# Optimization experiments

Measured on AMD Instinct MI355X. Metric: run time of the kernel, lower is better.

The kernel has to match this reference:

```python
import jax, jax.numpy as jnp
import numpy as np

C = 19          # EEG channels
NP = C * C      # 361 channel pairs
D = 256         # UNIFIED_FEATURE_DIM
H = 8           # num_heads
HD = D // H     # head dim


def _build_mask():
    # rel[p, q] = True iff key-pair q shares a channel with query-pair p
    idx = np.arange(NP)
    ci, cj = idx // C, idx % C
    rel = ((ci[:, None] == ci[None, :]) | (ci[:, None] == cj[None, :]) |
           (cj[:, None] == ci[None, :]) | (cj[:, None] == cj[None, :]))
    return jnp.asarray(rel.reshape(C, C, NP))  # (channel_i, j, key_pair)

MASK = _build_mask()


def setup_inputs() -> dict:
    key = jax.random.key(0)
    ks = jax.random.split(key, 6)
    s = 0.05
    return {
        "x": jax.random.normal(ks[0], (32, NP, D), jnp.float32),
        # 19 stacked nn.MultiheadAttention modules: in_proj (3D, D) = [Wq; Wk; Wv]
        "w_in": jax.random.normal(ks[1], (C, 3 * D, D), jnp.float32) * s,
        "b_in": jnp.zeros((C, 3 * D), jnp.float32),
        "w_out": jax.random.normal(ks[2], (C, D, D), jnp.float32) * s,
        "b_out": jnp.zeros((C, D), jnp.float32),
        # fusion: nn.Linear(D, D)
        "w_fuse": jax.random.normal(ks[3], (D, D), jnp.float32) * s,
        "b_fuse": jnp.zeros((D,), jnp.float32),
    }


def reference(x, w_in, b_in, w_out, b_out, w_fuse, b_fuse):
    # x: (B, 361, D). Pair p=(i,j) at index i*19+j uses attention module i,
    # query = x[:, p], keys/values = pairs sharing channel i or j (mask).
    B = x.shape[0]
    wq, wk, wv = w_in[:, :D], w_in[:, D:2 * D], w_in[:, 2 * D:]
    bq, bk, bv = b_in[:, :D], b_in[:, D:2 * D], b_in[:, 2 * D:]

    # Per-channel K/V projections over all 361 pairs: (C, B, NP, D)
    K = jnp.einsum('bnd,ced->cbne', x, wk) + bk[:, None, None, :]
    V = jnp.einsum('bnd,ced->cbne', x, wv) + bv[:, None, None, :]
    # Queries grouped by first channel i: x reshaped to (B, C, C, D)
    xq = x.reshape(B, C, C, D)
    Q = jnp.einsum('bcjd,ced->cbje', xq, wq) + bq[:, None, None, :]  # (C,B,C,D)

    Qh = Q.reshape(C, B, C, H, HD)
    Kh = K.reshape(C, B, NP, H, HD)
    Vh = V.reshape(C, B, NP, H, HD)

    scale = 1.0 / jnp.sqrt(jnp.asarray(HD, x.dtype))
    scores = jnp.einsum('cbqhe,cbkhe->cbhqk', Qh, Kh) * scale  # (C,B,H,C,NP)
    scores = jnp.where(MASK[:, None, None, :, :], scores, -jnp.inf)
    attn = jax.nn.softmax(scores, axis=-1)

    out = jnp.einsum('cbhqk,cbkhe->cbqhe', attn, Vh).reshape(C, B, C, D)
    out = jnp.einsum('cbqd,ced->cbqe', out, w_out) + b_out[:, None, None, :]
    out = out.transpose(1, 0, 2, 3).reshape(B, NP, D)  # back to (B, 361, D)

    # fusion ('linear') + residual
    return out @ w_fuse.T + b_fuse + x
```

## Files before the change

### kernel.cpp

```cpp
#include <hip/hip_runtime.h>

#define CC 19
#define NPOS 361
#define NPAD 384
#define DIM 256
#define TKEY 32
#define NTILES 12

#define LDS_BYTES 67584

using bf16x8 = __attribute__((ext_vector_type(8))) short;
using f16x4  = __attribute__((ext_vector_type(4))) _Float16;
using floatx4 = __attribute__((ext_vector_type(4))) float;
using uintx2 = __attribute__((ext_vector_type(2))) unsigned int;

__device__ __forceinline__ unsigned short f2bf(float f) {
  unsigned u = __builtin_bit_cast(unsigned, f);
  u += 0x7fffu + ((u >> 16) & 1u);
  return (unsigned short)(u >> 16);
}

__device__ __forceinline__ float bf2f(unsigned short h) {
  return __builtin_bit_cast(float, ((unsigned)h) << 16);
}

__device__ __forceinline__ f16x4 pack4h(float a, float b, float c2, float d) {
  const auto h01 = __builtin_amdgcn_cvt_pkrtz(a, b);
  const auto h23 = __builtin_amdgcn_cvt_pkrtz(c2, d);
  uintx2 uv = {__builtin_bit_cast(unsigned, h01), __builtin_bit_cast(unsigned, h23)};
  return __builtin_bit_cast(f16x4, uv);
}

__device__ __forceinline__ void gload_lds16(const void* g, void* l) {
  __builtin_amdgcn_global_load_lds(
      (const __attribute__((address_space(1))) void*)g,
      (__attribute__((address_space(3))) void*)l, 16, 0, 0);
}

__global__ void conv_all_kernel(const float* __restrict__ x,
                                const float* __restrict__ w_in,
                                const float* __restrict__ w_fuse,
                                unsigned short* __restrict__ ws) {
  const int j = blockIdx.x * 256 + threadIdx.x;
  float4 v = make_float4(0.f, 0.f, 0.f, 0.f);
  unsigned short* dst;
  if (j < 786432) {
    const int row = j >> 6;
    const int off = (j & 63) << 2;
    const int b = row / NPAD;
    const int r = row - b * NPAD;
    if (r < NPOS) v = *(const float4*)&x[(b * NPOS + r) * DIM + off];
    dst = &ws[row * DIM + off];
  } else if (j < 1720320) {
    const int k = j - 786432;
    v = *(const float4*)&w_in[k << 2];
    dst = &ws[3145728 + (k << 2)];
  } else {
    const int k = j - 1720320;
    v = *(const float4*)&w_fuse[k << 2];
    dst = &ws[8126464 + (k << 2)];
  }
  ushort4 o;
  o.x = f2bf(v.x); o.y = f2bf(v.y); o.z = f2bf(v.z); o.w = f2bf(v.w);
  *(ushort4*)dst = o;
}

__launch_bounds__(512)
__global__ void wcomb_kernel(const float* __restrict__ wof,
                             const unsigned short* __restrict__ wfbf,
                             unsigned short* __restrict__ wcbf) {
  const int c = blockIdx.x >> 2;
  const int fslab = blockIdx.x & 3;
  const int tid = threadIdx.x;
  const int w = tid >> 6;
  const int lane = tid & 63;
  const int quad = lane >> 4;
  const int l16 = lane & 15;

  const int f_w = fslab * 64 + (w & 3) * 16;
  const int d0_w = (w >> 2) * 128;
  const floatx4 fzero = {0.f, 0.f, 0.f, 0.f};

  floatx4 acc[8];
#pragma unroll
  for (int nt = 0; nt < 8; ++nt) acc[nt] = fzero;

  for (int kt = 0; kt < 8; ++kt) {
    const bf16x8 a8 = *(const bf16x8*)&wfbf[(f_w + l16) * 256 + kt * 32 + quad * 8];
#pragma unroll
    for (int nt = 0; nt < 8; ++nt) {
      const int d = d0_w + nt * 16 + l16;
      bf16x8 bn;
#pragma unroll
      for (int j = 0; j < 8; ++j) {
        const float v = wof[c * 65536 + (kt * 32 + quad * 8 + j) * 256 + d];
        bn[j] = (short)f2bf(v);
      }
      acc[nt] = __builtin_amdgcn_mfma_f32_16x16x32_bf16(a8, bn, acc[nt], 0, 0, 0);
    }
  }
#pragma unroll
  for (int nt = 0; nt < 8; ++nt)
#pragma unroll
    for (int r = 0; r < 4; ++r)
      wcbf[(c * 256 + f_w + quad * 4 + r) * 256 + d0_w + nt * 16 + l16] =
          f2bf(acc[nt][r]);
}

__launch_bounds__(256, 2)
__global__ void attn_kernel(const float* __restrict__ b_in,
                            const unsigned short* __restrict__ xbf,
                            const unsigned short* __restrict__ wibf,
                            float* __restrict__ out) {
  const int bid = blockIdx.x;
  const int xcd = bid & 7;
  const int slot = bid >> 3;
  const int c = slot >> 3;
  const int p = ((slot & 7) << 3) | xcd;
  const int b = p >> 1;
  const int hb = p & 1;

  const int tid = threadIdx.x;
  const int w = tid >> 6;
  const int lane = tid & 63;
  const int quad = lane >> 4;
  const int l16 = lane & 15;
  const int eh = (hb * 4 + w) * 32;

  extern __shared__ char smem[];
  char* sx = smem;
  unsigned* msk = (unsigned*)(smem + 65536);
  float* sL = (float*)(smem + 67072);

  const float scale = 0.25503486f;
  const floatx4 fzero = {0.f, 0.f, 0.f, 0.f};

  const int xw = (l16 & 7) << 4;
  const size_t xrowbytes = (size_t)b * NPAD * 512;

#pragma unroll
  for (int u = 0; u < 2; ++u) {
#pragma unroll
    for (int call = 0; call < 4; ++call) {
      const int sbyte = w * 4096 + call * 1024 + (lane << 4);
      const int row = sbyte >> 9;
      const int inner = (sbyte & 511) ^ ((row & 7) << 4);
      gload_lds16((const char*)xbf + xrowbytes + (size_t)(u * TKEY + row) * 512 + inner,
                  sx + u * 16384 + w * 4096 + call * 1024);
    }
  }

  f16x4 qf[2][2];
  {
    bf16x8 wq[2][8];
#pragma unroll
    for (int m4 = 0; m4 < 2; ++m4)
#pragma unroll
      for (int k = 0; k < 8; ++k)
        wq[m4][k] = *(const bf16x8*)&wibf[(c * 768 + eh + m4 * 16 + l16) * DIM + k * 32 + quad * 8];
    float bq[2][4];
#pragma unroll
    for (int m4 = 0; m4 < 2; ++m4) {
      const float4 bv4 = *(const float4*)&b_in[c * 768 + eh + m4 * 16 + quad * 4];
      bq[m4][0] = bv4.x; bq[m4][1] = bv4.y; bq[m4][2] = bv4.z; bq[m4][3] = bv4.w;
    }
#pragma unroll
    for (int mt = 0; mt < 2; ++mt) {
      const int xrow = b * NPAD + c * CC + mt * 16 + l16;
      bf16x8 xq[8];
#pragma unroll
      for (int k = 0; k < 8; ++k)
        xq[k] = *(const bf16x8*)&xbf[xrow * DIM + k * 32 + quad * 8];
#pragma unroll
      for (int m4 = 0; m4 < 2; ++m4) {
        floatx4 acc = fzero;
#pragma unroll
        for (int k = 0; k < 8; ++k)
          acc = __builtin_amdgcn_mfma_f32_16x16x32_bf16(wq[m4][k], xq[k], acc, 0, 0, 0);
        qf[mt][m4] = pack4h((acc[0] + bq[m4][0]) * scale, (acc[1] + bq[m4][1]) * scale,
                            (acc[2] + bq[m4][2]) * scale, (acc[3] + bq[m4][3]) * scale);
      }
    }
  }

  bf16x8 wk[2][8], wv[2][8];
#pragma unroll
  for (int m4 = 0; m4 < 2; ++m4)
#pragma unroll
    for (int k = 0; k < 8; ++k) {
      wk[m4][k] =
          *(const bf16x8*)&wibf[(c * 768 + 256 + eh + m4 * 16 + l16) * DIM + k * 32 + quad * 8];
      wv[m4][k] =
          *(const bf16x8*)&wibf[(c * 768 + 512 + eh + m4 * 16 + l16) * DIM + k * 32 + quad * 8];
    }
  float bV[2];
#pragma unroll
  for (int ne = 0; ne < 2; ++ne) bV[ne] = b_in[c * 768 + 512 + eh + ne * 16 + l16];

  for (int e2 = tid; e2 < 384; e2 += 256) {
    const int q = e2 / 12;
    const int wd = e2 - q * 12;
    unsigned m = 0u;
    for (int i = 0; i < 32; ++i) {
      const int kabs = wd * 32 + i;
      const unsigned ki = ((unsigned)kabs * 110377u) >> 21;
      const unsigned kj = (unsigned)kabs - ki * 19u;
      if (kabs < NPOS && (ki == (unsigned)c || kj == (unsigned)c ||
                          ki == (unsigned)q || kj == (unsigned)q))
        m |= (1u << i);
    }
    msk[e2] = m;
  }

  floatx4 o_acc[2][2];
  float lsum[2] = {0.f, 0.f};
#pragma unroll
  for (int mt = 0; mt < 2; ++mt)
#pragma unroll
    for (int ne = 0; ne < 2; ++ne) o_acc[mt][ne] = fzero;

  __syncthreads();

  for (int s6 = 0; s6 < 6; ++s6) {
    const int tb = s6 * 2;
    if (s6 < 5) {
#pragma unroll
      for (int u = 0; u < 2; ++u) {
        const int t = tb + 2 + u;
        char* bxn = sx + (t & 3) * 16384;
#pragma unroll
        for (int call = 0; call < 4; ++call) {
          const int sbyte = w * 4096 + call * 1024 + (lane << 4);
          const int row = sbyte >> 9;
          const int inner = (sbyte & 511) ^ ((row & 7) << 4);
          gload_lds16((const char*)xbf + xrowbytes + (size_t)(t * TKEY + row) * 512 + inner,
                      bxn + w * 4096 + call * 1024);
        }
      }
    }

#pragma unroll
    for (int u = 0; u < 2; ++u) {
      const int t = tb + u;
      const char* bx = sx + (t & 3) * 16384;

      floatx4 aK[2][2], aV[2][2];
#pragma unroll
      for (int i = 0; i < 2; ++i)
#pragma unroll
        for (int j = 0; j < 2; ++j) { aK[i][j] = fzero; aV[i][j] = fzero; }
      __builtin_amdgcn_s_setprio(1);
#pragma unroll
      for (int k = 0; k < 8; ++k) {
        bf16x8 xfr[2];
#pragma unroll
        for (int n4 = 0; n4 < 2; ++n4) {
          const int row = n4 * 16 + l16;
          const int inner = (k * 64 + quad * 16) ^ xw;
          xfr[n4] = *(const bf16x8*)(bx + row * 512 + inner);
        }
#pragma unroll
        for (int m4 = 0; m4 < 2; ++m4)
#pragma unroll
          for (int n4 = 0; n4 < 2; ++n4) {
            aK[m4][n4] = __builtin_amdgcn_mfma_f32_16x16x32_bf16(wk[m4][k], xfr[n4], aK[m4][n4], 0, 0, 0);
            aV[n4][m4] = __builtin_amdgcn_mfma_f32_16x16x32_bf16(xfr[n4], wv[m4][k], aV[n4][m4], 0, 0, 0);
          }
      }
      __builtin_amdgcn_s_setprio(0);

      f16x4 kf[2][2];
      f16x4 vf[2][2];
#pragma unroll
      for (int kt = 0; kt < 2; ++kt)
#pragma unroll
        for (int ec = 0; ec < 2; ++ec) {
          kf[kt][ec] = pack4h(aK[ec][kt][0], aK[ec][kt][1], aK[ec][kt][2], aK[ec][kt][3]);
          vf[kt][ec] = pack4h(aV[kt][ec][0], aV[kt][ec][1], aV[kt][ec][2], aV[kt][ec][3]);
        }

#pragma unroll
      for (int mt = 0; mt < 2; ++mt) {
        const int q = mt * 16 + l16;
        const unsigned mw = msk[q * 12 + t];
        f16x4 pf[2];
#pragma unroll
        for (int kt = 0; kt < 2; ++kt) {
          floatx4 s2 = __builtin_amdgcn_mfma_f32_16x16x16f16(kf[kt][0], qf[mt][0], fzero, 0, 0, 0);
          s2 = __builtin_amdgcn_mfma_f32_16x16x16f16(kf[kt][1], qf[mt][1], s2, 0, 0, 0);
          const unsigned mk = mw >> (kt * 16 + quad * 4);
          float p[4];
#pragma unroll
          for (int r = 0; r < 4; ++r)
            p[r] = (mk & (1u << r)) ? __builtin_exp2f(s2[r]) : 0.f;
          lsum[mt] += (p[0] + p[1]) + (p[2] + p[3]);
          pf[kt] = pack4h(p[0], p[1], p[2], p[3]);
        }
        __builtin_amdgcn_s_setprio(1);
#pragma unroll
        for (int kt = 0; kt < 2; ++kt)
#pragma unroll
          for (int ne = 0; ne < 2; ++ne)
            o_acc[mt][ne] =
                __builtin_amdgcn_mfma_f32_16x16x16f16(pf[kt], vf[kt][ne], o_acc[mt][ne], 0, 0, 0);
        __builtin_amdgcn_s_setprio(0);
      }
    }
    if (s6 < 5) __syncthreads();
  }

#pragma unroll
  for (int mt = 0; mt < 2; ++mt) {
    lsum[mt] += __shfl_xor(lsum[mt], 16);
    lsum[mt] += __shfl_xor(lsum[mt], 32);
  }
  if (lane < 16) {
    sL[w * 32 + lane] = lsum[0];
    sL[w * 32 + 16 + lane] = lsum[1];
  }
  float invl[2][4];
#pragma unroll
  for (int mt = 0; mt < 2; ++mt)
#pragma unroll
    for (int r = 0; r < 4; ++r)
      invl[mt][r] = 1.f / sL[w * 32 + mt * 16 + quad * 4 + r];

  unsigned short* aop = (unsigned short*)(out + (size_t)(b * NPOS + c * CC) * DIM);
#pragma unroll
  for (int mt = 0; mt < 2; ++mt)
#pragma unroll
    for (int ne = 0; ne < 2; ++ne)
#pragma unroll
      for (int r = 0; r < 4; ++r) {
        const int q = mt * 16 + quad * 4 + r;
        if (q < CC)
          aop[q * DIM + eh + ne * 16 + l16] =
              f2bf(o_acc[mt][ne][r] * invl[mt][r] + bV[ne]);
      }
}

__launch_bounds__(512)
__global__ void epi_kernel(const float* __restrict__ xf,
                           const float* __restrict__ b_out,
                           const float* __restrict__ b_fuse,
                           const unsigned short* __restrict__ wfbf,
                           const unsigned short* __restrict__ wcbf,
                           float* __restrict__ out) {
  const int bid = blockIdx.x;
  const int xcd = bid & 7;
  const int slot = bid >> 3;
  const int c = slot >> 2;
  const int b = ((slot & 3) << 3) | xcd;

  const int tid = threadIdx.x;
  const int w = tid >> 6;
  const int lane = tid & 63;
  const int quad = lane >> 4;
  const int l16 = lane & 15;

  __shared__ unsigned short sA[32 * 264];

  const size_t fbase = (size_t)(b * NPOS + c * CC) * DIM;
  const unsigned short* aop = (const unsigned short*)(out + fbase);
  const floatx4 fzero = {0.f, 0.f, 0.f, 0.f};
  const bf16x8 zero8 = {};

#pragma unroll
  for (int it = 0; it < 2; ++it) {
    const int cc2 = tid + it * 512;
    const int row = cc2 >> 5;
    const int col = (cc2 & 31) * 8;
    bf16x8 v = zero8;
    if (row < CC) v = *(const bf16x8*)&aop[row * DIM + col];
    *(bf16x8*)&sA[row * 264 + col] = v;
  }

  float bc[2];
#pragma unroll
  for (int nt2 = 0; nt2 < 2; ++nt2) {
    const int f = w * 32 + nt2 * 16 + l16;
    float s = b_fuse[f];
    for (int kk = 0; kk < 32; ++kk) {
      const bf16x8 w8 = *(const bf16x8*)&wfbf[f * 256 + kk * 8];
#pragma unroll
      for (int j = 0; j < 8; ++j)
        s += bf2f((unsigned short)w8[j]) * b_out[c * 256 + kk * 8 + j];
    }
    bc[nt2] = s;
  }
  __syncthreads();

#pragma unroll
  for (int mt = 0; mt < 2; ++mt) {
    bf16x8 a8[8];
#pragma unroll
    for (int k = 0; k < 8; ++k)
      a8[k] = *(const bf16x8*)&sA[(mt * 16 + l16) * 264 + k * 32 + quad * 8];
#pragma unroll
    for (int nt2 = 0; nt2 < 2; ++nt2) {
      const int e0 = w * 32 + nt2 * 16;
      floatx4 acc = fzero;
#pragma unroll
      for (int k = 0; k < 8; ++k) {
        bf16x8 b8 = *(const bf16x8*)&wcbf[(c * 256 + e0 + l16) * DIM + k * 32 + quad * 8];
        acc = __builtin_amdgcn_mfma_f32_16x16x32_bf16(a8[k], b8, acc, 0, 0, 0);
      }
#pragma unroll
      for (int r = 0; r < 4; ++r) {
        const int row = mt * 16 + quad * 4 + r;
        if (row < CC) {
          const size_t gp = fbase + (size_t)row * DIM + e0 + l16;
          out[gp] = acc[r] + bc[nt2] + xf[gp];
        }
      }
    }
  }
}

extern "C" void kernel_launch(void* const* d_in, const int* in_sizes, int n_in,
                              void* d_out, int out_size, void* d_ws, size_t ws_size,
                              hipStream_t stream) {
  const float* x      = (const float*)d_in[0];
  const float* w_in   = (const float*)d_in[1];
  const float* b_in   = (const float*)d_in[2];
  const float* w_out  = (const float*)d_in[3];
  const float* b_out  = (const float*)d_in[4];
  const float* w_fuse = (const float*)d_in[5];
  const float* b_fuse = (const float*)d_in[6];
  float* out = (float*)d_out;

  if (ws_size < (size_t)16384000) return;

  unsigned short* ws = (unsigned short*)d_ws;
  unsigned short* x_bf  = ws;
  unsigned short* wi_bf = ws + 3145728;
  unsigned short* wc_bf = ws + 6881280;
  unsigned short* wf_bf = ws + 8126464;

  conv_all_kernel<<<6784, 256, 0, stream>>>(x, w_in, w_fuse, ws);

  wcomb_kernel<<<76, 512, 0, stream>>>(w_out, wf_bf, wc_bf);

  (void)hipFuncSetAttribute((const void*)attn_kernel,
                            hipFuncAttributeMaxDynamicSharedMemorySize, LDS_BYTES);
  attn_kernel<<<1216, 256, LDS_BYTES, stream>>>(b_in, x_bf, wi_bf, out);

  epi_kernel<<<608, 512, 0, stream>>>(x, b_out, b_fuse, wf_bf, wc_bf, out);
}
```

Baseline: 255.3 us.

## Fuse weight-combine into prep kernel and split epilogue across feature halves

Merges the bf16 conversion kernel and the W_fuse·W_out combine kernel into a single prep launch. The combine becomes a plain fp32 FMA loop over 608 extra blocks rather than a separate 76-block MFMA kernel with strided loads. This removes one launch and the serial dependency, and spreads the combine over many more blocks. The epilogue is retiled to 256-thread blocks, each handling half of the output features, so twice as many blocks run. The trade-off is that the fp32 combine does more scalar loads and FMAs, and each epilogue block reloads the same A tile.

```diff
diff --git a/kernel.cpp b/kernel.cpp
--- a/kernel.cpp
+++ b/kernel.cpp
@@ -37,74 +37,65 @@
       (__attribute__((address_space(3))) void*)l, 16, 0, 0);
 }
 
-__global__ void conv_all_kernel(const float* __restrict__ x,
-                                const float* __restrict__ w_in,
-                                const float* __restrict__ w_fuse,
-                                unsigned short* __restrict__ ws) {
-  const int j = blockIdx.x * 256 + threadIdx.x;
-  float4 v = make_float4(0.f, 0.f, 0.f, 0.f);
-  unsigned short* dst;
-  if (j < 786432) {
-    const int row = j >> 6;
-    const int off = (j & 63) << 2;
-    const int b = row / NPAD;
-    const int r = row - b * NPAD;
-    if (r < NPOS) v = *(const float4*)&x[(b * NPOS + r) * DIM + off];
-    dst = &ws[row * DIM + off];
-  } else if (j < 1720320) {
-    const int k = j - 786432;
-    v = *(const float4*)&w_in[k << 2];
-    dst = &ws[3145728 + (k << 2)];
+__global__ void prep_kernel(const float* __restrict__ x,
+                            const float* __restrict__ w_in,
+                            const float* __restrict__ w_fuse,
+                            const float* __restrict__ w_out,
+                            unsigned short* __restrict__ ws) {
+  if (blockIdx.x < 6784) {
+    const int j = blockIdx.x * 256 + threadIdx.x;
+    float4 v = make_float4(0.f, 0.f, 0.f, 0.f);
+    unsigned short* dst;
+    if (j < 786432) {
+      const int row = j >> 6;
+      const int off = (j & 63) << 2;
+      const int b = row / NPAD;
+      const int r = row - b * NPAD;
+      if (r < NPOS) v = *(const float4*)&x[(b * NPOS + r) * DIM + off];
+      dst = &ws[row * DIM + off];
+    } else if (j < 1720320) {
+      const int k = j - 786432;
+      v = *(const float4*)&w_in[k << 2];
+      dst = &ws[3145728 + (k << 2)];
+    } else {
+      const int k = j - 1720320;
+      v = *(const float4*)&w_fuse[k << 2];
+      dst = &ws[8126464 + (k << 2)];
+    }
+    ushort4 o;
+    o.x = f2bf(v.x); o.y = f2bf(v.y); o.z = f2bf(v.z); o.w = f2bf(v.w);
+    *(ushort4*)dst = o;
   } else {
-    const int k = j - 1720320;
-    v = *(const float4*)&w_fuse[k << 2];
-    dst = &ws[8126464 + (k << 2)];
-  }
-  ushort4 o;
-  o.x = f2bf(v.x); o.y = f2bf(v.y); o.z = f2bf(v.z); o.w = f2bf(v.w);
-  *(ushort4*)dst = o;
-}
-
-__launch_bounds__(512)
-__global__ void wcomb_kernel(const float* __restrict__ wof,
-                             const unsigned short* __restrict__ wfbf,
-                             unsigned short* __restrict__ wcbf) {
-  const int c = blockIdx.x >> 2;
-  const int fslab = blockIdx.x & 3;
-  const int tid = threadIdx.x;
-  const int w = tid >> 6;
-  const int lane = tid & 63;
-  const int quad = lane >> 4;
-  const int l16 = lane & 15;
-
-  const int f_w = fslab * 64 + (w & 3) * 16;
-  const int d0_w = (w >> 2) * 128;
-  const floatx4 fzero = {0.f, 0.f, 0.f, 0.f};
-
-  floatx4 acc[8];
-#pragma unroll
-  for (int nt = 0; nt < 8; ++nt) acc[nt] = fzero;
-
-  for (int kt = 0; kt < 8; ++kt) {
-    const bf16x8 a8 = *(const bf16x8*)&wfbf[(f_w + l16) * 256 + kt * 32 + quad * 8];
-#pragma unroll
-    for (int nt = 0; nt < 8; ++nt) {
-      const int d = d0_w + nt * 16 + l16;
-      bf16x8 bn;
-#pragma unroll
-      for (int j = 0; j < 8; ++j) {
-        const float v = wof[c * 65536 + (kt * 32 + quad * 8 + j) * 256 + d];
-        bn[j] = (short)f2bf(v);
-      }
-      acc[nt] = __builtin_amdgcn_mfma_f32_16x16x32_bf16(a8, bn, acc[nt], 0, 0, 0);
-    }
-  }
-#pragma unroll
-  for (int nt = 0; nt < 8; ++nt)
-#pragma unroll
-    for (int r = 0; r < 4; ++r)
-      wcbf[(c * 256 + f_w + quad * 4 + r) * 256 + d0_w + nt * 16 + l16] =
-          f2bf(acc[nt][r]);
+    const int wb = blockIdx.x - 6784;
+    const int c = wb >> 5;
+    const int fg = wb & 31;
+    const int fl = threadIdx.x >> 5;
+    const int dq = threadIdx.x & 31;
+    const int f = fg * 8 + fl;
+
+    const float* wfrow = w_fuse + f * 256;
+    const float* wo = w_out + c * 65536 + dq * 8;
+
+    floatx4 accA = {0.f, 0.f, 0.f, 0.f};
+    floatx4 accB = {0.f, 0.f, 0.f, 0.f};
+    for (int ec = 0; ec < 64; ++ec) {
+      const floatx4 wf4 = *(const floatx4*)&wfrow[ec * 4];
+#pragma unroll
+      for (int i = 0; i < 4; ++i) {
+        const int e = ec * 4 + i;
+        const floatx4 a = *(const floatx4*)&wo[e * 256];
+        const floatx4 b2 = *(const floatx4*)&wo[e * 256 + 4];
+        accA += wf4[i] * a;
+        accB += wf4[i] * b2;
+      }
+    }
+    unsigned short* dst = &ws[6881280 + (c * 256 + f) * 256 + dq * 8];
+    ushort4 o1, o2;
+    o1.x = f2bf(accA[0]); o1.y = f2bf(accA[1]); o1.z = f2bf(accA[2]); o1.w = f2bf(accA[3]);
+    o2.x = f2bf(accB[0]); o2.y = f2bf(accB[1]); o2.z = f2bf(accB[2]); o2.w = f2bf(accB[3]);
+    *(ushort4*)dst = o1;
+    *(ushort4*)(dst + 4) = o2;
+  }
 }
 
 __launch_bounds__(256, 2)
@@ -339,7 +330,7 @@
       }
 }
 
-__launch_bounds__(512)
+__launch_bounds__(256)
 __global__ void epi_kernel(const float* __restrict__ xf,
                            const float* __restrict__ b_out,
                            const float* __restrict__ b_fuse,
@@ -349,8 +340,10 @@
   const int bid = blockIdx.x;
   const int xcd = bid & 7;
   const int slot = bid >> 3;
-  const int c = slot >> 2;
-  const int b = ((slot & 3) << 3) | xcd;
+  const int c = slot >> 3;
+  const int p = ((slot & 7) << 3) | xcd;
+  const int b = p >> 1;
+  const int fh = p & 1;
 
   const int tid = threadIdx.x;
   const int w = tid >> 6;
@@ -366,8 +359,8 @@
   const bf16x8 zero8 = {};
 
 #pragma unroll
-  for (int it = 0; it < 2; ++it) {
-    const int cc2 = tid + it * 512;
+  for (int it = 0; it < 4; ++it) {
+    const int cc2 = tid + it * 256;
     const int row = cc2 >> 5;
     const int col = (cc2 & 31) * 8;
     bf16x8 v = zero8;
@@ -378,7 +371,7 @@
   float bc[2];
 #pragma unroll
   for (int nt2 = 0; nt2 < 2; ++nt2) {
-    const int f = w * 32 + nt2 * 16 + l16;
+    const int f = fh * 128 + w * 32 + nt2 * 16 + l16;
     float s = b_fuse[f];
     for (int kk = 0; kk < 32; ++kk) {
       const bf16x8 w8 = *(const bf16x8*)&wfbf[f * 256 + kk * 8];
@@ -398,7 +391,7 @@
       a8[k] = *(const bf16x8*)&sA[(mt * 16 + l16) * 264 + k * 32 + quad * 8];
 #pragma unroll
     for (int nt2 = 0; nt2 < 2; ++nt2) {
-      const int e0 = w * 32 + nt2 * 16;
+      const int e0 = fh * 128 + w * 32 + nt2 * 16;
       floatx4 acc = fzero;
 #pragma unroll
       for (int k = 0; k < 8; ++k) {
@@ -437,13 +430,11 @@
   unsigned short* wc_bf = ws + 6881280;
   unsigned short* wf_bf = ws + 8126464;
 
-  conv_all_kernel<<<6784, 256, 0, stream>>>(x, w_in, w_fuse, ws);
-
-  wcomb_kernel<<<76, 512, 0, stream>>>(w_out, wf_bf, wc_bf);
+  prep_kernel<<<7392, 256, 0, stream>>>(x, w_in, w_fuse, w_out, ws);
 
   (void)hipFuncSetAttribute((const void*)attn_kernel,
                             hipFuncAttributeMaxDynamicSharedMemorySize, LDS_BYTES);
   attn_kernel<<<1216, 256, LDS_BYTES, stream>>>(b_in, x_bf, wi_bf, out);
 
-  epi_kernel<<<608, 512, 0, stream>>>(x, b_out, b_fuse, wf_bf, wc_bf, out);
-}
+  epi_kernel<<<1216, 256, 0, stream>>>(x, b_out, b_fuse, wf_bf, wc_bf, out);
+}
```

Measured after the change: 357.9 us. +40.2%, slower.
